# Kernel tuning notes

Hardware: AMD Instinct MI355X
Metric: run time of the kernel (lower is better)

The kernel has to match this reference:

```python
import jax, jax.numpy as jnp
import numpy as np
from jax import lax

LRELU_SLOPE = 0.2
EPS = 1e-8


def eq_linear(x, W, b):
    # EqualizedLinear: weight scaled by 1/sqrt(fan_in)
    c = 1.0 / np.sqrt(W.shape[1])
    return x @ (W * c).T + b


def mod_conv(x, s, W, demod):
    # x: [b, cin, h, w], s: [b, cin], W: [cout, cin, k, k]
    b, cin, h, w = x.shape
    cout, _, k, _ = W.shape
    c = 1.0 / np.sqrt(cin * k * k)
    weights = (W * c)[None] * s[:, None, :, None, None]  # [b, cout, cin, k, k]
    if demod:
        sigma_inv = lax.rsqrt(jnp.sum(weights ** 2, axis=(2, 3, 4)) + EPS)  # [b, cout]
        weights = weights * sigma_inv[:, :, None, None, None]
    x2 = x.reshape(1, b * cin, h, w)
    wk = weights.reshape(b * cout, cin, k, k)
    pad = k // 2
    out = lax.conv_general_dilated(
        x2, wk, window_strides=(1, 1), padding=[(pad, pad), (pad, pad)],
        dimension_numbers=("NCHW", "OIHW", "NCHW"), feature_group_count=b)
    return out.reshape(b, cout, h, w)


def style_block(x, w, noise, style_W, style_b, conv_W, scale_noise, bias):
    A = eq_linear(w, style_W, style_b)          # [b, cin]
    x = mod_conv(x, A, conv_W, demod=True)      # [b, cout, h, w]
    if noise is not None:
        x = x + scale_noise[None, :, None, None] * noise
    return jax.nn.leaky_relu(x + bias[None, :, None, None], LRELU_SLOPE)


def rgb_block(x, w, style_W, style_b, conv_W, bias):
    A = eq_linear(w, style_W, style_b)
    x = mod_conv(x, A, conv_W, demod=False)     # 1x1 conv to 3 channels
    return jax.nn.leaky_relu(x + bias[None, :, None, None], LRELU_SLOPE)


def setup_inputs() -> dict:
    key = jax.random.key(0)
    ks = jax.random.split(key, 10)
    B, CIN, COUT, WD, H, W = 8, 512, 512, 512, 64, 64
    return {
        "x": jax.random.normal(ks[0], (B, CIN, H, W), jnp.float32),
        "w": jax.random.normal(ks[1], (B, WD), jnp.float32),
        "noise": jax.random.normal(ks[2], (2, B, 1, H, W), jnp.float32),
        # StyleBlock 1
        "s1_style_W": jax.random.normal(ks[3], (CIN, WD), jnp.float32),
        "s1_style_b": jnp.ones((CIN,), jnp.float32),
        "s1_conv_W": jax.random.normal(ks[4], (COUT, CIN, 3, 3), jnp.float32),
        "s1_scale_noise": jnp.zeros((1,), jnp.float32),
        "s1_bias": jnp.zeros((COUT,), jnp.float32),
        # StyleBlock 2
        "s2_style_W": jax.random.normal(ks[5], (COUT, WD), jnp.float32),
        "s2_style_b": jnp.ones((COUT,), jnp.float32),
        "s2_conv_W": jax.random.normal(ks[6], (COUT, COUT, 3, 3), jnp.float32),
        "s2_scale_noise": jnp.zeros((1,), jnp.float32),
        "s2_bias": jnp.zeros((COUT,), jnp.float32),
        # RGBBlock
        "rgb_style_W": jax.random.normal(ks[7], (COUT, WD), jnp.float32),
        "rgb_style_b": jnp.ones((COUT,), jnp.float32),
        "rgb_conv_W": jax.random.normal(ks[8], (3, COUT, 1, 1), jnp.float32),
        "rgb_bias": jnp.zeros((3,), jnp.float32),
    }


def reference(x, w, noise,
              s1_style_W, s1_style_b, s1_conv_W, s1_scale_noise, s1_bias,
              s2_style_W, s2_style_b, s2_conv_W, s2_scale_noise, s2_bias,
              rgb_style_W, rgb_style_b, rgb_conv_W, rgb_bias):
    x = style_block(x, w, noise[0], s1_style_W, s1_style_b, s1_conv_W, s1_scale_noise, s1_bias)
    x = style_block(x, w, noise[1], s2_style_W, s2_style_b, s2_conv_W, s2_scale_noise, s2_bias)
    rgb = rgb_block(x, w, rgb_style_W, rgb_style_b, rgb_conv_W, rgb_bias)
    return (x, rgb)
```

## Files before the change

kernel.cpp:

```cpp
#include <hip/hip_runtime.h>
#include <stdint.h>

typedef __attribute__((ext_vector_type(8))) short bf16x8;
typedef __attribute__((ext_vector_type(4))) float f32x4;

__device__ __forceinline__ ushort f2bf(float f) {
  uint32_t u = __builtin_bit_cast(uint32_t, f);
  u += 0x7fffu + ((u >> 16) & 1u);
  return (ushort)(u >> 16);
}

__device__ __forceinline__ void async_copy16(const void* gsrc, void* ldst) {
  __builtin_amdgcn_global_load_lds(
      (const __attribute__((address_space(1))) void*)gsrc,
      (__attribute__((address_space(3))) void*)ldst, 16, 0, 0);
}

__global__ void style_linear(const float* __restrict__ w, const float* __restrict__ sW,
                             const float* __restrict__ sb, float* __restrict__ A) {
  const int b = blockIdx.y;
  const int lane = threadIdx.x & 63, wv = threadIdx.x >> 6;
  const int co = blockIdx.x * 4 + wv;
  const float c = 0.04419417382415922f;
  const float* wr = w + b * 512;
  const float* Wr = sW + (size_t)co * 512;
  float s = 0.f;
#pragma unroll
  for (int i = 0; i < 8; ++i) {
    const int d = i * 64 + lane;
    s += wr[d] * Wr[d];
  }
#pragma unroll
  for (int off = 32; off; off >>= 1) s += __shfl_xor(s, off);
  if (lane == 0) A[b * 512 + co] = s * c + sb[co];
}

__global__ void prep_sigma(const float* __restrict__ Wc, const float* __restrict__ A,
                           ushort* __restrict__ Wt, float* __restrict__ sig) {
  const int co = blockIdx.x;
  const int ci = threadIdx.x;
  const int lane = ci & 63, wid = ci >> 6;
  const float c = 0.014731391274719738f;
  const float* src = Wc + ((size_t)co * 512 + ci) * 9;
  float s = 0.f;
#pragma unroll
  for (int t = 0; t < 9; ++t) {
    float v = src[t] * c;
    Wt[(size_t)t * 262144 + co * 512 + ci] = f2bf(v);
    s += v * v;
  }
  __shared__ float red[8][8];
#pragma unroll
  for (int b = 0; b < 8; ++b) {
    float a = A[b * 512 + ci];
    float v = s * a * a;
#pragma unroll
    for (int off = 32; off; off >>= 1) v += __shfl_xor(v, off);
    if (lane == 0) red[b][wid] = v;
  }
  __syncthreads();
  if (ci < 8) {
    float t = 0.f;
#pragma unroll
    for (int wv = 0; wv < 8; ++wv) t += red[ci][wv];
    sig[ci * 512 + co] = rsqrtf(t + 1e-8f);
  }
}

__global__ void zero_border(uint4* __restrict__ x1, uint4* __restrict__ x2) {
  const int i = blockIdx.x * 256 + threadIdx.x;
  const int per = 16640;
  const int tot = per * 8;
  if (i >= 2 * tot) return;
  uint4* base = (i < tot) ? x1 : x2;
  int t = (i < tot) ? i : i - tot;
  const int bb = t / per;
  int r = t - bb * per;
  int row, cell, q;
  if (r < 8448) {
    row = (r >= 4224) ? 65 : 0;
    int pos = (r >= 4224) ? r - 4224 : r;
    cell = pos >> 6;
    q = pos & 63;
  } else {
    int r2 = r - 8448;
    row = 1 + (r2 >> 7);
    cell = ((r2 >> 6) & 1) ? 65 : 0;
    q = r2 & 63;
  }
  base[(((size_t)bb * 66 + row) * 66 + cell) * 64 + q] = make_uint4(0u, 0u, 0u, 0u);
}

__global__ void mod_transpose(const float* __restrict__ X, const float* __restrict__ A,
                              ushort* __restrict__ xs) {
  __shared__ float tile[128][65];
  const int h = blockIdx.x;
  const int ci0 = blockIdx.y * 128;
  const int b = blockIdx.z;
  const int tid = threadIdx.x;
  const int wcol = tid & 63;
  const int r0 = tid >> 6;
#pragma unroll 4
  for (int i = 0; i < 32; ++i) {
    const int cil = r0 + i * 4;
    const int ci = ci0 + cil;
    const size_t off = ((size_t)(b * 512 + ci) * 64 + h) * 64 + wcol;
    tile[cil][wcol] = X[off] * A[b * 512 + ci];
  }
  __syncthreads();
  const int sub = tid & 3;
  const int w = tid >> 2;
  ushort* dst = xs + (((size_t)b * 66 + (h + 1)) * 66 + (w + 1)) * 512 + ci0 + sub * 32;
#pragma unroll
  for (int g = 0; g < 4; ++g) {
    bf16x8 v;
#pragma unroll
    for (int j = 0; j < 8; ++j) v[j] = (short)f2bf(tile[sub * 32 + g * 8 + j][w]);
    *(bf16x8*)(dst + g * 8) = v;
  }
}

#define WAITVM(N) asm volatile("s_waitcnt vmcnt(" #N ")" ::: "memory")

#define READS(S, AF, BV)                                                     \
  do {                                                                       \
    const int q_ = (S) & 3;                                                  \
    const char* baA = (const char*)(&smA[0][0] + q_ * 8192);                 \
    const char* baB = (const char*)(&smB[0][0] + q_ * 8192);                 \
    _Pragma("unroll") for (int m_ = 0; m_ < 8; ++m_)                         \
        AF[m_] = *(const bf16x8*)(baA + aro[m_]);                            \
    _Pragma("unroll") for (int n_ = 0; n_ < 4; ++n_)                         \
        BV[n_] = *(const bf16x8*)(baB + bro[n_]);                            \
  } while (0)

#define PH(S, WN, DOREAD, DOSTAGE, RAF, RBV, MAF, MBV)                               \
  do {                                                                               \
    WAITVM(WN);                                                                      \
    asm volatile("" ::: "memory");                                                   \
    __builtin_amdgcn_s_barrier();                                                    \
    asm volatile("" ::: "memory");                                                   \
    if (DOREAD) READS((S) + 1, RAF, RBV);                                            \
    if (DOSTAGE) stage((S) + 3);                                                     \
    __builtin_amdgcn_sched_barrier(0);                                               \
    __builtin_amdgcn_s_setprio(1);                                                   \
    _Pragma("unroll") for (int m_ = 0; m_ < 8; ++m_)                                 \
      _Pragma("unroll") for (int n_ = 0; n_ < 4; ++n_)                               \
        acc[m_][n_] = __builtin_amdgcn_mfma_f32_16x16x32_bf16(MAF[m_], MBV[n_],      \
                                                              acc[m_][n_], 0, 0, 0); \
    __builtin_amdgcn_s_setprio(0);                                                   \
    __builtin_amdgcn_sched_barrier(0);                                               \
  } while (0)

template <int OUT_MODE>
__global__ __launch_bounds__(512, 2) void conv3x3(
    const ushort* __restrict__ xs, const ushort* __restrict__ Wt,
    const float* __restrict__ sig, const float* __restrict__ noise,
    const float* __restrict__ scale_noise, const float* __restrict__ bias,
    const float* __restrict__ amod, void* __restrict__ outp) {
  __shared__ __align__(16) ushort smA[4][8192];
  __shared__ __align__(16) ushort smB[4][8192];
  const int tid = threadIdx.x, lane = tid & 63, wid = tid >> 6;
  const int wr = wid >> 2, wc = wid & 3;
  const int id = blockIdx.x;
  const int b = id & 7;
  const int tile = id >> 3;
  const int co0 = (tile & 1) * 256;
  const int px0 = (tile >> 1) * 256;
  const int h0 = px0 >> 6;

  const int sswz = ((lane & 3) ^ ((lane >> 3) & 3)) * 8;
  int aoff[2], boff[2];
  ushort *ldsA[2], *ldsB[2];
#pragma unroll
  for (int i = 0; i < 2; ++i) {
    const int row = (i * 8 + wid) * 16 + (lane >> 2);
    aoff[i] = (co0 + row) * 512 + sswz;
    const int hh = h0 + (row >> 6), ww = row & 63;
    boff[i] = ((b * 66 + hh) * 66 + ww) * 512 + sswz;
    ldsA[i] = &smA[0][0] + (i * 8 + wid) * 512 + lane * 8;
    ldsB[i] = &smB[0][0] + (i * 8 + wid) * 512 + lane * 8;
  }
  const int rdsw = ((lane >> 4) ^ ((lane >> 1) & 3)) * 16;
  int aro[8], bro[4];
#pragma unroll
  for (int m = 0; m < 8; ++m) aro[m] = (wr * 128 + m * 16 + (lane & 15)) * 64 + rdsw;
#pragma unroll
  for (int n = 0; n < 4; ++n) bro[n] = (wc * 64 + n * 16 + (lane & 15)) * 64 + rdsw;

  f32x4 acc[8][4];
#pragma unroll
  for (int m = 0; m < 8; ++m)
#pragma unroll
    for (int n = 0; n < 4; ++n) acc[m][n] = (f32x4){0.f, 0.f, 0.f, 0.f};

  auto stage = [&](int s) {
    const int tap = s >> 4;
    const int ci0 = (s & 15) << 5;
    const int kh = tap / 3;
    const int kw = tap - kh * 3;
    const int q = s & 3;
    const ushort* Wb = Wt + tap * 262144 + ci0;
    const ushort* Xb = xs + (kh * 66 + kw) * 512 + ci0;
    async_copy16(Wb + aoff[0], ldsA[0] + q * 8192);
    async_copy16(Wb + aoff[1], ldsA[1] + q * 8192);
    async_copy16(Xb + boff[0], ldsB[0] + q * 8192);
    async_copy16(Xb + boff[1], ldsB[1] + q * 8192);
  };

  bf16x8 afA[8], bvA[4], afB[8], bvB[4];

  stage(0);
  stage(1);
  stage(2);
  WAITVM(8);
  __builtin_amdgcn_s_barrier();
  READS(0, afA, bvA);

  for (int s = 0; s < 140; s += 2) {
    PH(s, 4, true, true, afB, bvB, afA, bvA);
    PH(s + 1, 4, true, true, afA, bvA, afB, bvB);
  }
  PH(140, 4, true, true, afB, bvB, afA, bvA);
  PH(141, 4, true, false, afA, bvA, afB, bvB);
  PH(142, 0, true, false, afB, bvB, afA, bvA);
  PH(143, 0, false, false, afA, bvA, afB, bvB);

  const float sn = scale_noise[0];
  const int colp = lane & 15;
  const int rq = (lane >> 4) * 4;
  float nz[4];
#pragma unroll
  for (int n = 0; n < 4; ++n)
    nz[n] = sn * noise[b * 4096 + px0 + wc * 64 + n * 16 + colp];
#pragma unroll
  for (int m = 0; m < 8; ++m) {
    const int cob = co0 + wr * 128 + m * 16 + rq;
    float sg[4], bs[4], am[4];
#pragma unroll
    for (int r = 0; r < 4; ++r) {
      sg[r] = sig[b * 512 + cob + r];
      bs[r] = bias[cob + r];
      am[r] = (OUT_MODE == 0) ? amod[b * 512 + cob + r] : 0.f;
    }
#pragma unroll
    for (int n = 0; n < 4; ++n) {
      const int px = px0 + wc * 64 + n * 16 + colp;
      if (OUT_MODE == 0) {
        const int hh = px >> 6, ww = px & 63;
        ushort pk[4];
#pragma unroll
        for (int r = 0; r < 4; ++r) {
          float v = acc[m][n][r] * sg[r] + nz[n] + bs[r];
          v = (v > 0.f) ? v : 0.2f * v;
          pk[r] = f2bf(v * am[r]);
        }
        uint2 u;
        u.x = (uint32_t)pk[0] | ((uint32_t)pk[1] << 16);
        u.y = (uint32_t)pk[2] | ((uint32_t)pk[3] << 16);
        *(uint2*)((ushort*)outp + (((size_t)b * 66 + hh + 1) * 66 + (ww + 1)) * 512 + cob) = u;
      } else {
#pragma unroll
        for (int r = 0; r < 4; ++r) {
          float v = acc[m][n][r] * sg[r] + nz[n] + bs[r];
          v = (v > 0.f) ? v : 0.2f * v;
          ((float*)outp)[((size_t)b * 512 + cob + r) * 4096 + px] = v;
        }
      }
    }
  }
}

__global__ void rgb_k(const float* __restrict__ X, const float* __restrict__ Ar,
                      const float* __restrict__ rgbW, const float* __restrict__ rgbB,
                      float* __restrict__ out) {
  __shared__ float wmod[3 * 512];
  const int b = blockIdx.y;
  const int tid = threadIdx.x;
  const float c = 0.04419417382415922f;
  for (int idx = tid; idx < 1536; idx += 256)
    wmod[idx] = rgbW[idx] * c * Ar[b * 512 + (idx & 511)];
  __syncthreads();
  const int p = blockIdx.x * 256 + tid;
  const float* xb = X + (size_t)b * 512 * 4096 + p;
  float a0 = 0.f, a1 = 0.f, a2 = 0.f;
  for (int ci = 0; ci < 512; ++ci) {
    float xv = xb[(size_t)ci * 4096];
    a0 += wmod[ci] * xv;
    a1 += wmod[512 + ci] * xv;
    a2 += wmod[1024 + ci] * xv;
  }
  float v0 = a0 + rgbB[0], v1 = a1 + rgbB[1], v2 = a2 + rgbB[2];
  v0 = (v0 > 0.f) ? v0 : 0.2f * v0;
  v1 = (v1 > 0.f) ? v1 : 0.2f * v1;
  v2 = (v2 > 0.f) ? v2 : 0.2f * v2;
  out[((size_t)b * 3 + 0) * 4096 + p] = v0;
  out[((size_t)b * 3 + 1) * 4096 + p] = v1;
  out[((size_t)b * 3 + 2) * 4096 + p] = v2;
}

extern "C" void kernel_launch(void* const* d_in, const int* in_sizes, int n_in,
                              void* d_out, int out_size, void* d_ws, size_t ws_size,
                              hipStream_t stream) {
  const float* x     = (const float*)d_in[0];
  const float* w     = (const float*)d_in[1];
  const float* noise = (const float*)d_in[2];
  const float* s1_sW = (const float*)d_in[3];
  const float* s1_sb = (const float*)d_in[4];
  const float* s1_cW = (const float*)d_in[5];
  const float* s1_sn = (const float*)d_in[6];
  const float* s1_b  = (const float*)d_in[7];
  const float* s2_sW = (const float*)d_in[8];
  const float* s2_sb = (const float*)d_in[9];
  const float* s2_cW = (const float*)d_in[10];
  const float* s2_sn = (const float*)d_in[11];
  const float* s2_b  = (const float*)d_in[12];
  const float* r_sW  = (const float*)d_in[13];
  const float* r_sb  = (const float*)d_in[14];
  const float* r_cW  = (const float*)d_in[15];
  const float* r_b   = (const float*)d_in[16];

  char* ws = (char*)d_ws;
  float*  A1  = (float*)(ws + 0);
  float*  A2  = (float*)(ws + 16384);
  float*  Arr = (float*)(ws + 32768);
  float*  sg1 = (float*)(ws + 49152);
  float*  sg2 = (float*)(ws + 65536);
  ushort* Wt1 = (ushort*)(ws + 98304);
  ushort* xs1 = (ushort*)(ws + 4816896);
  ushort* Wt2 = (ushort*)(ws + 4816896);
  ushort* xs2 = (ushort*)(ws + 40501248);
  float* outx   = (float*)d_out;
  float* outrgb = outx + (size_t)8 * 512 * 4096;

  style_linear<<<dim3(128, 8), 256, 0, stream>>>(w, s1_sW, s1_sb, A1);
  style_linear<<<dim3(128, 8), 256, 0, stream>>>(w, s2_sW, s2_sb, A2);
  style_linear<<<dim3(128, 8), 256, 0, stream>>>(w, r_sW, r_sb, Arr);

  prep_sigma<<<512, 512, 0, stream>>>(s1_cW, A1, Wt1, sg1);

  zero_border<<<1040, 256, 0, stream>>>((uint4*)xs1, (uint4*)xs2);
  mod_transpose<<<dim3(64, 4, 8), 256, 0, stream>>>(x, A1, xs1);

  conv3x3<0><<<dim3(256), 512, 0, stream>>>(xs1, Wt1, sg1, noise, s1_sn, s1_b, A2, (void*)xs2);
  prep_sigma<<<512, 512, 0, stream>>>(s2_cW, A2, Wt2, sg2);
  conv3x3<1><<<dim3(256), 512, 0, stream>>>(xs2, Wt2, sg2, noise + 32768, s2_sn, s2_b, sg2,
                                            (void*)outx);
  rgb_k<<<dim3(16, 8), 256, 0, stream>>>(outx, Arr, r_cW, r_b, outrgb);
}
```

Before: 340.0 us.

## Load conv weights directly into registers and fuse RGB projection into conv epilogue

```diff
diff --git a/kernel.cpp b/kernel.cpp
--- a/kernel.cpp
+++ b/kernel.cpp
@@ -46,7 +46,7 @@
 #pragma unroll
   for (int t = 0; t < 9; ++t) {
     float v = src[t] * c;
-    Wt[(size_t)t * 262144 + co * 512 + ci] = f2bf(v);
+    Wt[((size_t)t * 16 + (ci >> 5)) * 16384 + co * 32 + (ci & 31)] = f2bf(v);
     s += v * v;
   }
   __shared__ float red[8][8];
@@ -67,11 +67,16 @@
   }
 }
 
-__global__ void zero_border(uint4* __restrict__ x1, uint4* __restrict__ x2) {
+__global__ void zero_border(uint4* __restrict__ x1, uint4* __restrict__ x2,
+                            uint4* __restrict__ rgb) {
   const int i = blockIdx.x * 256 + threadIdx.x;
   const int per = 16640;
   const int tot = per * 8;
-  if (i >= 2 * tot) return;
+  if (i >= 2 * tot) {
+    const int j = i - 2 * tot;
+    if (j < 24576) rgb[j] = make_uint4(0u, 0u, 0u, 0u);
+    return;
+  }
   uint4* base = (i < tot) ? x1 : x2;
   int t = (i < tot) ? i : i - tot;
   const int bb = t / per;
@@ -122,13 +127,16 @@
 
 #define WAITVM(N) asm volatile("s_waitcnt vmcnt(" #N ")" ::: "memory")
 
-#define READS(S, AF, BV)                                                     \
+#define ALOAD(S, AF)                                                         \
   do {                                                                       \
-    const int q_ = (S) & 3;                                                  \
-    const char* baA = (const char*)(&smA[0][0] + q_ * 8192);                 \
-    const char* baB = (const char*)(&smB[0][0] + q_ * 8192);                 \
+    const ushort* Ag_ = WtA + (size_t)(S) * 16384;                           \
     _Pragma("unroll") for (int m_ = 0; m_ < 8; ++m_)                         \
-        AF[m_] = *(const bf16x8*)(baA + aro[m_]);                            \
+        AF[m_] = *(const bf16x8*)(Ag_ + AoffL[m_]);                          \
+  } while (0)
+
+#define READB(S, BV)                                                         \
+  do {                                                                       \
+    const char* baB = (const char*)(&smB[0][0] + ((S) & 3) * 8192);          \
     _Pragma("unroll") for (int n_ = 0; n_ < 4; ++n_)                         \
         BV[n_] = *(const bf16x8*)(baB + bro[n_]);                            \
   } while (0)
@@ -139,8 +147,11 @@
     asm volatile("" ::: "memory");                                                   \
     __builtin_amdgcn_s_barrier();                                                    \
     asm volatile("" ::: "memory");                                                   \
-    if (DOREAD) READS((S) + 1, RAF, RBV);                                            \
     if (DOSTAGE) stage((S) + 3);                                                     \
+    if (DOREAD) {                                                                    \
+      ALOAD((S) + 1, RAF);                                                           \
+      READB((S) + 1, RBV);                                                           \
+    }                                                                                \
     __builtin_amdgcn_sched_barrier(0);                                               \
     __builtin_amdgcn_s_setprio(1);                                                   \
     _Pragma("unroll") for (int m_ = 0; m_ < 8; ++m_)                                 \
@@ -156,8 +167,9 @@
     const ushort* __restrict__ xs, const ushort* __restrict__ Wt,
     const float* __restrict__ sig, const float* __restrict__ noise,
     const float* __restrict__ scale_noise, const float* __restrict__ bias,
-    const float* __restrict__ amod, void* __restrict__ outp) {
-  __shared__ __align__(16) ushort smA[4][8192];
+    const float* __restrict__ amod, void* __restrict__ outp,
+    const float* __restrict__ rgbw, const float* __restrict__ arr,
+    float* __restrict__ outrgb) {
   __shared__ __align__(16) ushort smB[4][8192];
   const int tid = threadIdx.x, lane = tid & 63, wid = tid >> 6;
   const int wr = wid >> 2, wc = wid & 3;
@@ -169,23 +181,24 @@
   const int h0 = px0 >> 6;
 
   const int sswz = ((lane & 3) ^ ((lane >> 3) & 3)) * 8;
-  int aoff[2], boff[2];
-  ushort *ldsA[2], *ldsB[2];
+  int boff[2];
+  ushort* ldsB[2];
 #pragma unroll
   for (int i = 0; i < 2; ++i) {
     const int row = (i * 8 + wid) * 16 + (lane >> 2);
-    aoff[i] = (co0 + row) * 512 + sswz;
     const int hh = h0 + (row >> 6), ww = row & 63;
     boff[i] = ((b * 66 + hh) * 66 + ww) * 512 + sswz;
-    ldsA[i] = &smA[0][0] + (i * 8 + wid) * 512 + lane * 8;
     ldsB[i] = &smB[0][0] + (i * 8 + wid) * 512 + lane * 8;
   }
   const int rdsw = ((lane >> 4) ^ ((lane >> 1) & 3)) * 16;
-  int aro[8], bro[4];
-#pragma unroll
-  for (int m = 0; m < 8; ++m) aro[m] = (wr * 128 + m * 16 + (lane & 15)) * 64 + rdsw;
+  int bro[4];
 #pragma unroll
   for (int n = 0; n < 4; ++n) bro[n] = (wc * 64 + n * 16 + (lane & 15)) * 64 + rdsw;
+  const ushort* WtA = Wt + co0 * 32;
+  int AoffL[8];
+#pragma unroll
+  for (int m = 0; m < 8; ++m)
+    AoffL[m] = (wr * 128 + m * 16 + (lane & 15)) * 32 + (lane >> 4) * 8;
 
   f32x4 acc[8][4];
 #pragma unroll
@@ -199,10 +212,7 @@
     const int kh = tap / 3;
     const int kw = tap - kh * 3;
     const int q = s & 3;
-    const ushort* Wb = Wt + tap * 262144 + ci0;
     const ushort* Xb = xs + (kh * 66 + kw) * 512 + ci0;
-    async_copy16(Wb + aoff[0], ldsA[0] + q * 8192);
-    async_copy16(Wb + aoff[1], ldsA[1] + q * 8192);
     async_copy16(Xb + boff[0], ldsB[0] + q * 8192);
     async_copy16(Xb + boff[1], ldsB[1] + q * 8192);
   };
@@ -212,18 +222,19 @@
   stage(0);
   stage(1);
   stage(2);
-  WAITVM(8);
+  ALOAD(0, afA);
+  WAITVM(12);
   __builtin_amdgcn_s_barrier();
-  READS(0, afA, bvA);
+  READB(0, bvA);
 
   for (int s = 0; s < 140; s += 2) {
-    PH(s, 4, true, true, afB, bvB, afA, bvA);
-    PH(s + 1, 4, true, true, afA, bvA, afB, bvB);
-  }
-  PH(140, 4, true, true, afB, bvB, afA, bvA);
-  PH(141, 4, true, false, afA, bvA, afB, bvB);
-  PH(142, 0, true, false, afB, bvB, afA, bvA);
-  PH(143, 0, false, false, afA, bvA, afB, bvB);
+    PH(s, 10, true, true, afB, bvB, afA, bvA);
+    PH(s + 1, 10, true, true, afA, bvA, afB, bvB);
+  }
+  PH(140, 10, true, true, afB, bvB, afA, bvA);
+  PH(141, 10, true, false, afA, bvA, afB, bvB);
+  PH(142, 8, true, false, afB, bvB, afA, bvA);
+  PH(143, 8, false, false, afA, bvA, afB, bvB);
 
   const float sn = scale_noise[0];
   const int colp = lane & 15;
@@ -232,15 +243,28 @@
 #pragma unroll
   for (int n = 0; n < 4; ++n)
     nz[n] = sn * noise[b * 4096 + px0 + wc * 64 + n * 16 + colp];
+  float rgbp[3][4];
+#pragma unroll
+  for (int c = 0; c < 3; ++c)
+#pragma unroll
+    for (int n = 0; n < 4; ++n) rgbp[c][n] = 0.f;
 #pragma unroll
   for (int m = 0; m < 8; ++m) {
     const int cob = co0 + wr * 128 + m * 16 + rq;
     float sg[4], bs[4], am[4];
+    float w0[4], w1[4], w2[4];
 #pragma unroll
     for (int r = 0; r < 4; ++r) {
       sg[r] = sig[b * 512 + cob + r];
       bs[r] = bias[cob + r];
-      am[r] = (OUT_MODE == 0) ? amod[b * 512 + cob + r] : 0.f;
+      if (OUT_MODE == 0) {
+        am[r] = amod[b * 512 + cob + r];
+      } else {
+        const float a3 = arr[b * 512 + cob + r] * 0.04419417382415922f;
+        w0[r] = rgbw[cob + r] * a3;
+        w1[r] = rgbw[512 + cob + r] * a3;
+        w2[r] = rgbw[1024 + cob + r] * a3;
+      }
     }
 #pragma unroll
     for (int n = 0; n < 4; ++n) {
@@ -264,38 +288,33 @@
           float v = acc[m][n][r] * sg[r] + nz[n] + bs[r];
           v = (v > 0.f) ? v : 0.2f * v;
           ((float*)outp)[((size_t)b * 512 + cob + r) * 4096 + px] = v;
+          rgbp[0][n] += w0[r] * v;
+          rgbp[1][n] += w1[r] * v;
+          rgbp[2][n] += w2[r] * v;
         }
       }
     }
   }
-}
-
-__global__ void rgb_k(const float* __restrict__ X, const float* __restrict__ Ar,
-                      const float* __restrict__ rgbW, const float* __restrict__ rgbB,
-                      float* __restrict__ out) {
-  __shared__ float wmod[3 * 512];
-  const int b = blockIdx.y;
-  const int tid = threadIdx.x;
-  const float c = 0.04419417382415922f;
-  for (int idx = tid; idx < 1536; idx += 256)
-    wmod[idx] = rgbW[idx] * c * Ar[b * 512 + (idx & 511)];
-  __syncthreads();
-  const int p = blockIdx.x * 256 + tid;
-  const float* xb = X + (size_t)b * 512 * 4096 + p;
-  float a0 = 0.f, a1 = 0.f, a2 = 0.f;
-  for (int ci = 0; ci < 512; ++ci) {
-    float xv = xb[(size_t)ci * 4096];
-    a0 += wmod[ci] * xv;
-    a1 += wmod[512 + ci] * xv;
-    a2 += wmod[1024 + ci] * xv;
-  }
-  float v0 = a0 + rgbB[0], v1 = a1 + rgbB[1], v2 = a2 + rgbB[2];
-  v0 = (v0 > 0.f) ? v0 : 0.2f * v0;
-  v1 = (v1 > 0.f) ? v1 : 0.2f * v1;
-  v2 = (v2 > 0.f) ? v2 : 0.2f * v2;
-  out[((size_t)b * 3 + 0) * 4096 + p] = v0;
-  out[((size_t)b * 3 + 1) * 4096 + p] = v1;
-  out[((size_t)b * 3 + 2) * 4096 + p] = v2;
+  if (OUT_MODE == 1) {
+#pragma unroll
+    for (int c = 0; c < 3; ++c)
+#pragma unroll
+      for (int n = 0; n < 4; ++n) {
+        float s = rgbp[c][n];
+        s += __shfl_xor(s, 16);
+        s += __shfl_xor(s, 32);
+        if (lane < 16)
+          atomicAdd(&outrgb[((size_t)b * 3 + c) * 4096 + px0 + wc * 64 + n * 16 + colp], s);
+      }
+  }
+}
+
+__global__ void rgb_finish(float* __restrict__ o, const float* __restrict__ rb) {
+  const int i = blockIdx.x * 256 + threadIdx.x;
+  if (i >= 98304) return;
+  const int c = (i >> 12) % 3;
+  float v = o[i] + rb[c];
+  o[i] = (v > 0.f) ? v : 0.2f * v;
 }
 
 extern "C" void kernel_launch(void* const* d_in, const int* in_sizes, int n_in,
@@ -338,12 +357,13 @@
 
   prep_sigma<<<512, 512, 0, stream>>>(s1_cW, A1, Wt1, sg1);
 
-  zero_border<<<1040, 256, 0, stream>>>((uint4*)xs1, (uint4*)xs2);
+  zero_border<<<1136, 256, 0, stream>>>((uint4*)xs1, (uint4*)xs2, (uint4*)outrgb);
   mod_transpose<<<dim3(64, 4, 8), 256, 0, stream>>>(x, A1, xs1);
 
-  conv3x3<0><<<dim3(256), 512, 0, stream>>>(xs1, Wt1, sg1, noise, s1_sn, s1_b, A2, (void*)xs2);
+  conv3x3<0><<<dim3(256), 512, 0, stream>>>(xs1, Wt1, sg1, noise, s1_sn, s1_b, A2, (void*)xs2,
+                                            r_cW, Arr, outrgb);
   prep_sigma<<<512, 512, 0, stream>>>(s2_cW, A2, Wt2, sg2);
   conv3x3<1><<<dim3(256), 512, 0, stream>>>(xs2, Wt2, sg2, noise + 32768, s2_sn, s2_b, sg2,
-                                            (void*)outx);
-  rgb_k<<<dim3(16, 8), 256, 0, stream>>>(outx, Arr, r_cW, r_b, outrgb);
-}
+                                            (void*)outx, r_cW, Arr, outrgb);
+  rgb_finish<<<384, 256, 0, stream>>>(outrgb, r_b);
+}
```

Result: slower. 472.2 us (+38.9%).
